# Kernel tuning notes

Measured on AMD Instinct MI355X. Metric: run time of the kernel, lower is better.

The kernel has to match this reference:

```python
import jax, jax.numpy as jnp
import numpy as np

STD_SEP2 = 0.05 ** 2  # 0.0025
COEF = -0.001 / STD_SEP2  # -0.4


def setup_inputs() -> dict:
    key = jax.random.key(0)
    keypoints = jax.random.uniform(key, (64, 8192, 2), dtype=jnp.float32)
    return {"keypoints": keypoints}


def reference(keypoints):
    B, N, C = keypoints.shape
    # Original computes, for each pair (i, j), i != j:
    #   d_ij = sqrt( sum over batch AND coords of (K[:,i,:] - K[:,j,:])**2 )
    #   loss += exp(-0.001 * d_ij / std_sep^2)
    # i.e. a Frobenius norm over the full [B, C] slice per keypoint pair.
    # Flatten each keypoint's [B, C] slice into a row vector -> [N, B*C],
    # then use the ||a||^2 + ||b||^2 - 2 a.b trick for all pairwise distances.
    X = jnp.transpose(keypoints, (1, 0, 2)).reshape(N, B * C)  # [N, B*C]
    sq = jnp.sum(X * X, axis=1)                                # [N]
    d2 = sq[:, None] + sq[None, :] - 2.0 * (X @ X.T)           # [N, N]
    eye = jnp.eye(N, dtype=bool)
    # guard diagonal / tiny negatives before sqrt (exact zeros would NaN grads)
    d2_safe = jnp.maximum(jnp.where(eye, 1.0, d2), 0.0)
    d = jnp.sqrt(d2_safe)
    loss = jnp.sum(jnp.where(eye, 0.0, jnp.exp(COEF * d)))
    return loss
```

## Files before the change

kernel.cpp:

```cpp
#include <hip/hip_runtime.h>
#include <hip/hip_bf16.h>


#define N_KP   8192
#define KDIM   128
#define NT     64
#define NTILES (NT * (NT + 1) / 2)
#define COEF2  (-0.57707801635558535f)

typedef __attribute__((ext_vector_type(8))) short bf16x8;
typedef __attribute__((ext_vector_type(4))) float f32x4;


__device__ __forceinline__ unsigned short f2bf(float f) {
    unsigned int u = __builtin_bit_cast(unsigned int, f);
    unsigned int r = (u + 0x7FFFu + ((u >> 16) & 1u)) >> 16;
    return (unsigned short)r;
}

__device__ __forceinline__ float bf2f(unsigned short u) {
    unsigned int x = ((unsigned int)u) << 16;
    return __builtin_bit_cast(float, x);
}

__device__ __forceinline__ void gload_lds16(const void* g, void* l) {
    __builtin_amdgcn_global_load_lds(
        (const __attribute__((address_space(1))) unsigned int*)g,
        (__attribute__((address_space(3))) unsigned int*)l, 16, 0, 0);
}

__global__ __launch_bounds__(256) void prep_kernel(
        const float* __restrict__ in, unsigned short* __restrict__ Xbf,
        float* __restrict__ sq) {
    int tid = threadIdx.x;
    int p = tid >> 5, idx = tid & 31;
    int n = blockIdx.x * 32 + idx;
    int t16 = n >> 4, l16 = n & 15;
    unsigned int* dst = (unsigned int*)Xbf;
    float s = 0.0f;
    #pragma unroll
    for (int q = 0; q < 8; ++q) {
        int b = p * 8 + q;
        float2 v = *(const float2*)(in + (size_t)b * (N_KP * 2) + n * 2);
        unsigned short h0 = f2bf(v.x);
        unsigned short h1 = f2bf(v.y);
        float f0 = bf2f(h0), f1 = bf2f(h1);
        s = fmaf(f0, f0, s);
        s = fmaf(f1, f1, s);
        unsigned int off_us = (((unsigned)(t16 * 4 + (b >> 4)) * 64
                                + ((b >> 2) & 3) * 16 + l16) << 3) + ((b & 3) << 1);
        dst[off_us >> 1] = ((unsigned int)h1 << 16) | h0;
    }
    __shared__ float wsq[256];
    wsq[tid] = s;
    __syncthreads();
    if (tid < 32) {
        float t = 0.0f;
        #pragma unroll
        for (int pp = 0; pp < 8; ++pp) t += wsq[pp * 32 + tid];
        sq[blockIdx.x * 32 + tid] = t;
    }
}

__global__ __launch_bounds__(256, 4) void pair_kernel(
        const unsigned short* __restrict__ Xbf, const float* __restrict__ sq,
        float* __restrict__ partials) {
    int bid = blockIdx.x;
    int ti = (int)((129.0f - sqrtf(129.0f * 129.0f - 8.0f * (float)bid)) * 0.5f);
    while (ti > 0 && ti * (129 - ti) / 2 > bid) --ti;
    while ((ti + 1) * (129 - (ti + 1)) / 2 <= bid) ++ti;
    int tj = ti + (bid - ti * (129 - ti) / 2);

    int wid  = threadIdx.x >> 6;
    int lane = threadIdx.x & 63;
    int wr = wid >> 1, wc = wid & 1;
    int l16 = lane & 15, lhi = lane >> 4;

    __shared__ __align__(16) unsigned short B_lds[32 * 512];
    __shared__ float wsum[4];

    #pragma unroll
    for (int c0 = 0; c0 < 8; ++c0) {
        int c = wid * 8 + c0;
        gload_lds16((const char*)Xbf + ((size_t)(tj * 32 + c)) * 1024 + lane * 16,
                    (char*)B_lds + (size_t)c * 1024);
    }
    __syncthreads();

    const bf16x8* Xs8 = (const bf16x8*)Xbf;
    const bf16x8* L   = (const bf16x8*)B_lds;

    f32x4 acc[4][4] = {};
    #pragma unroll
    for (int kk = 0; kk < 4; ++kk) {
        bf16x8 a[4], b[4];
        #pragma unroll
        for (int m = 0; m < 4; ++m)
            a[m] = Xs8[(size_t)((ti * 8 + wr * 4 + m) * 4 + kk) * 64 + lane];
        #pragma unroll
        for (int n = 0; n < 4; ++n)
            b[n] = L[((wc * 4 + n) * 4 + kk) * 64 + lane];
        #pragma unroll
        for (int m = 0; m < 4; ++m)
            #pragma unroll
            for (int n = 0; n < 4; ++n)
                acc[m][n] = __builtin_amdgcn_mfma_f32_16x16x32_bf16(
                    a[m], b[n], acc[m][n], 0, 0, 0);
    }

    int ibase = ti * 128 + wr * 64;
    int jbase = tj * 128 + wc * 64;

    float si[4][4];
    #pragma unroll
    for (int m = 0; m < 4; ++m)
        #pragma unroll
        for (int r = 0; r < 4; ++r)
            si[m][r] = sq[ibase + m * 16 + lhi * 4 + r];
    float sqj[4];
    #pragma unroll
    for (int n = 0; n < 4; ++n) sqj[n] = sq[jbase + n * 16 + l16];

    float p0 = 0.0f, p1 = 0.0f, p2 = 0.0f, p3 = 0.0f;
    #pragma unroll
    for (int m = 0; m < 4; ++m) {
        #pragma unroll
        for (int n = 0; n < 4; ++n) {
            float d2_0 = fmaf(-2.0f, acc[m][n][0], si[m][0] + sqj[n]);
            float d2_1 = fmaf(-2.0f, acc[m][n][1], si[m][1] + sqj[n]);
            float d2_2 = fmaf(-2.0f, acc[m][n][2], si[m][2] + sqj[n]);
            float d2_3 = fmaf(-2.0f, acc[m][n][3], si[m][3] + sqj[n]);
            p0 += __builtin_amdgcn_exp2f(COEF2 * __builtin_amdgcn_sqrtf(fabsf(d2_0)));
            p1 += __builtin_amdgcn_exp2f(COEF2 * __builtin_amdgcn_sqrtf(fabsf(d2_1)));
            p2 += __builtin_amdgcn_exp2f(COEF2 * __builtin_amdgcn_sqrtf(fabsf(d2_2)));
            p3 += __builtin_amdgcn_exp2f(COEF2 * __builtin_amdgcn_sqrtf(fabsf(d2_3)));
        }
    }
    float partial = (p0 + p1) + (p2 + p3);

    #pragma unroll
    for (int m = 32; m; m >>= 1) partial += __shfl_xor(partial, m, 64);
    if (lane == 0) wsum[wid] = partial;
    __syncthreads();
    if (threadIdx.x == 0) {
        float v = (wsum[0] + wsum[1]) + (wsum[2] + wsum[3]);
        if (ti == tj) v -= 128.0f; else v *= 2.0f;
        partials[bid] = v;
    }
}

__global__ __launch_bounds__(256) void reduce_kernel(
        const float* __restrict__ partials, float* __restrict__ out) {
    float s = 0.0f;
    for (int i = threadIdx.x; i < NTILES; i += 256) s += partials[i];
    #pragma unroll
    for (int m = 32; m; m >>= 1) s += __shfl_xor(s, m, 64);
    __shared__ float wsum[4];
    int wid = threadIdx.x >> 6, lane = threadIdx.x & 63;
    if (lane == 0) wsum[wid] = s;
    __syncthreads();
    if (threadIdx.x == 0) out[0] = (wsum[0] + wsum[1]) + (wsum[2] + wsum[3]);
}

extern "C" void kernel_launch(void* const* d_in, const int* in_sizes, int n_in,
                              void* d_out, int out_size, void* d_ws, size_t ws_size,
                              hipStream_t stream) {
    const float* in = (const float*)d_in[0];
    float* out = (float*)d_out;

    unsigned short* Xbf = (unsigned short*)d_ws;
    float* sq = (float*)((char*)d_ws + (size_t)N_KP * KDIM * 2);
    float* partials = (float*)((char*)d_ws + (size_t)N_KP * KDIM * 2
                               + (size_t)N_KP * 4);

    prep_kernel<<<N_KP / 32, 256, 0, stream>>>(in, Xbf, sq);
    pair_kernel<<<NTILES, 256, 0, stream>>>(Xbf, sq, partials);
    reduce_kernel<<<1, 256, 0, stream>>>(partials, out);
}
```

Measured before the change: 31.87 us.

## Fuse final reduction into pair kernel, prefetch A fragments, widen prep grid

The separate reduce kernel is removed. The last pair block, found through an atomic counter with threadfence, now sums the partials and writes the output, which saves one kernel launch. The A-operand global loads are software-prefetched one k-step ahead, and the first load is issued before the LDS fill so it overlaps. The prep kernel now handles 16 keypoints per block, doubling its grid for more parallelism. In exchange, a memset of the counter is added to the stream, along with atomic and fence overhead in every block.

```diff
diff --git a/kernel.cpp b/kernel.cpp
--- a/kernel.cpp
+++ b/kernel.cpp
@@ -33,14 +33,14 @@
         const float* __restrict__ in, unsigned short* __restrict__ Xbf,
         float* __restrict__ sq) {
     int tid = threadIdx.x;
-    int p = tid >> 5, idx = tid & 31;
-    int n = blockIdx.x * 32 + idx;
+    int bt = tid >> 4, nl = tid & 15;
+    int n = blockIdx.x * 16 + nl;
     int t16 = n >> 4, l16 = n & 15;
     unsigned int* dst = (unsigned int*)Xbf;
     float s = 0.0f;
     #pragma unroll
-    for (int q = 0; q < 8; ++q) {
-        int b = p * 8 + q;
+    for (int q = 0; q < 4; ++q) {
+        int b = bt * 4 + q;
         float2 v = *(const float2*)(in + (size_t)b * (N_KP * 2) + n * 2);
         unsigned short h0 = f2bf(v.x);
         unsigned short h1 = f2bf(v.y);
@@ -54,17 +54,18 @@
     __shared__ float wsq[256];
     wsq[tid] = s;
     __syncthreads();
-    if (tid < 32) {
+    if (tid < 16) {
         float t = 0.0f;
         #pragma unroll
-        for (int pp = 0; pp < 8; ++pp) t += wsq[pp * 32 + tid];
-        sq[blockIdx.x * 32 + tid] = t;
+        for (int pp = 0; pp < 16; ++pp) t += wsq[pp * 16 + tid];
+        sq[blockIdx.x * 16 + tid] = t;
     }
 }
 
 __global__ __launch_bounds__(256, 4) void pair_kernel(
         const unsigned short* __restrict__ Xbf, const float* __restrict__ sq,
-        float* __restrict__ partials) {
+        float* __restrict__ partials, unsigned int* __restrict__ counter,
+        float* __restrict__ out) {
     int bid = blockIdx.x;
     int ti = (int)((129.0f - sqrtf(129.0f * 129.0f - 8.0f * (float)bid)) * 0.5f);
     while (ti > 0 && ti * (129 - ti) / 2 > bid) --ti;
@@ -78,6 +79,14 @@
 
     __shared__ __align__(16) unsigned short B_lds[32 * 512];
     __shared__ float wsum[4];
+    __shared__ int islast;
+
+    const bf16x8* Xs8 = (const bf16x8*)Xbf;
+
+    bf16x8 aN[4];
+    #pragma unroll
+    for (int m = 0; m < 4; ++m)
+        aN[m] = Xs8[(size_t)((ti * 8 + wr * 4 + m) * 4 + 0) * 64 + lane];
 
     #pragma unroll
     for (int c0 = 0; c0 < 8; ++c0) {
@@ -87,16 +96,20 @@
     }
     __syncthreads();
 
-    const bf16x8* Xs8 = (const bf16x8*)Xbf;
-    const bf16x8* L   = (const bf16x8*)B_lds;
+    const bf16x8* L = (const bf16x8*)B_lds;
 
     f32x4 acc[4][4] = {};
     #pragma unroll
     for (int kk = 0; kk < 4; ++kk) {
-        bf16x8 a[4], b[4];
+        bf16x8 aC[4];
         #pragma unroll
-        for (int m = 0; m < 4; ++m)
-            a[m] = Xs8[(size_t)((ti * 8 + wr * 4 + m) * 4 + kk) * 64 + lane];
+        for (int m = 0; m < 4; ++m) aC[m] = aN[m];
+        if (kk < 3) {
+            #pragma unroll
+            for (int m = 0; m < 4; ++m)
+                aN[m] = Xs8[(size_t)((ti * 8 + wr * 4 + m) * 4 + kk + 1) * 64 + lane];
+        }
+        bf16x8 b[4];
         #pragma unroll
         for (int n = 0; n < 4; ++n)
             b[n] = L[((wc * 4 + n) * 4 + kk) * 64 + lane];
@@ -105,7 +118,7 @@
             #pragma unroll
             for (int n = 0; n < 4; ++n)
                 acc[m][n] = __builtin_amdgcn_mfma_f32_16x16x32_bf16(
-                    a[m], b[n], acc[m][n], 0, 0, 0);
+                    aC[m], b[n], acc[m][n], 0, 0, 0);
     }
 
     int ibase = ti * 128 + wr * 64;
@@ -146,20 +159,24 @@
         float v = (wsum[0] + wsum[1]) + (wsum[2] + wsum[3]);
         if (ti == tj) v -= 128.0f; else v *= 2.0f;
         partials[bid] = v;
+        __threadfence();
+        unsigned int o = __hip_atomic_fetch_add(counter, 1u, __ATOMIC_ACQ_REL,
+                                                __HIP_MEMORY_SCOPE_AGENT);
+        islast = (o == NTILES - 1) ? 1 : 0;
     }
-}
+    __syncthreads();
 
-__global__ __launch_bounds__(256) void reduce_kernel(
-        const float* __restrict__ partials, float* __restrict__ out) {
-    float s = 0.0f;
-    for (int i = threadIdx.x; i < NTILES; i += 256) s += partials[i];
-    #pragma unroll
-    for (int m = 32; m; m >>= 1) s += __shfl_xor(s, m, 64);
-    __shared__ float wsum[4];
-    int wid = threadIdx.x >> 6, lane = threadIdx.x & 63;
-    if (lane == 0) wsum[wid] = s;
-    __syncthreads();
-    if (threadIdx.x == 0) out[0] = (wsum[0] + wsum[1]) + (wsum[2] + wsum[3]);
+    if (islast) {
+        __threadfence();
+        float s = 0.0f;
+        for (int i = threadIdx.x; i < NTILES; i += 256) s += partials[i];
+        #pragma unroll
+        for (int m = 32; m; m >>= 1) s += __shfl_xor(s, m, 64);
+        if (lane == 0) wsum[wid] = s;
+        __syncthreads();
+        if (threadIdx.x == 0)
+            out[0] = (wsum[0] + wsum[1]) + (wsum[2] + wsum[3]);
+    }
 }
 
 extern "C" void kernel_launch(void* const* d_in, const int* in_sizes, int n_in,
@@ -172,8 +189,9 @@
     float* sq = (float*)((char*)d_ws + (size_t)N_KP * KDIM * 2);
     float* partials = (float*)((char*)d_ws + (size_t)N_KP * KDIM * 2
                                + (size_t)N_KP * 4);
+    unsigned int* counter = (unsigned int*)(partials + NTILES);
 
-    prep_kernel<<<N_KP / 32, 256, 0, stream>>>(in, Xbf, sq);
-    pair_kernel<<<NTILES, 256, 0, stream>>>(Xbf, sq, partials);
-    reduce_kernel<<<1, 256, 0, stream>>>(partials, out);
+    hipMemsetAsync(counter, 0, sizeof(unsigned int), stream);
+    prep_kernel<<<N_KP / 16, 256, 0, stream>>>(in, Xbf, sq);
+    pair_kernel<<<NTILES, 256, 0, stream>>>(Xbf, sq, partials, counter, out);
 }
```

Measured after the change: 92.62 us. 2.91x slower.
